# Optimization experiments

Hardware: AMD Instinct MI355X
Metric: run time of the kernel (lower is better)

## Reference

```python
import jax, jax.numpy as jnp
import numpy as np

EMBED_DIM = 512
NUM_HEADS = 8
TGT_LEN = 2048
SRC_LEN = 2048
BSZ = 4
W_SCALE = 0.02  # keep pre-softmax logits in a sane range


def setup_inputs() -> dict:
    key = jax.random.key(0)
    ks = jax.random.split(key, 13)
    E = EMBED_DIM
    inp = {
        "query": jax.random.normal(ks[0], (TGT_LEN, BSZ, E), jnp.float32),
        "key": jax.random.normal(ks[1], (SRC_LEN, BSZ, E), jnp.float32),
        "value": jax.random.normal(ks[2], (SRC_LEN, BSZ, E), jnp.float32),
        "attn_mask": jax.random.normal(ks[3], (TGT_LEN, SRC_LEN), jnp.float32),
        # Linear params, torch layout: W is [out, in], y = x @ W.T + b
        "Wq": jax.random.normal(ks[4], (E, E), jnp.float32) * W_SCALE,
        "bq": jax.random.normal(ks[5], (E,), jnp.float32) * W_SCALE,
        "Wk": jax.random.normal(ks[6], (E, E), jnp.float32) * W_SCALE,
        "bk": jax.random.normal(ks[7], (E,), jnp.float32) * W_SCALE,
        "Wv": jax.random.normal(ks[8], (E, E), jnp.float32) * W_SCALE,
        "bv": jax.random.normal(ks[9], (E,), jnp.float32) * W_SCALE,
        "Wo": jax.random.normal(ks[10], (E, E), jnp.float32) * W_SCALE,
        "bo": jax.random.normal(ks[11], (E,), jnp.float32) * W_SCALE,
    }
    return inp


def reference(query, key, value, attn_mask, Wq, bq, Wk, bk, Wv, bv, Wo, bo):
    # QAT quant/dequant stubs are identity in float math; dropout p=0 (eval) is identity.
    T, B, E = query.shape
    S = key.shape[0]
    H = NUM_HEADS
    hd = E // H
    scale = hd ** (-0.5)

    q = query @ Wq.T + bq            # [T, B, E]
    k = key @ Wk.T + bk              # [S, B, E]
    v = value @ Wv.T + bv            # [S, B, E]

    q = q.reshape(T, B, H, hd) * scale
    k = k.reshape(S, B, H, hd)
    v = v.reshape(S, B, H, hd)

    # scores: [B, H, T, S]
    scores = jnp.einsum("tbhd,sbhd->bhts", q, k)
    scores = scores + attn_mask[None, None, :, :]  # mask_add.add (float mask)
    attn = jax.nn.softmax(scores, axis=-1)         # SegmentLUTSoftmax == softmax in float

    out = jnp.einsum("bhts,sbhd->tbhd", attn, v).reshape(T, B, E)
    out = out @ Wo.T + bo                          # out_proj

    # need_weights=True, average_attn_weights=True: mean over heads -> [B, T, S]
    attn_weights = jnp.sum(attn, axis=1) * (1.0 / H)
    return out, attn_weights
```

## Files before the change

### kernel.cpp

```cpp
#include <hip/hip_runtime.h>
#include <hip/hip_bf16.h>

#define T_LEN 2048
#define S_LEN 2048
#define BSZ   4
#define EMB   512
#define NHEAD 8
#define HDIM  64

using bf16x8 = __attribute__((ext_vector_type(8))) short;
using f32x4  = __attribute__((ext_vector_type(4))) float;

static __device__ __forceinline__ unsigned short f2bf(float x) {
    __hip_bfloat16 h = __float2bfloat16(x);
    return *reinterpret_cast<unsigned short*>(&h);
}
static __device__ __forceinline__ float bf2f(unsigned short u) {
    __hip_bfloat16 h;
    *reinterpret_cast<unsigned short*>(&h) = u;
    return __bfloat162float(h);
}
static __device__ __forceinline__ unsigned int pk2(float a, float b) {
    return (unsigned)f2bf(a) | ((unsigned)f2bf(b) << 16);
}

__global__ __launch_bounds__(256) void convert_w4(
    const float* __restrict__ W0, const float* __restrict__ W1,
    const float* __restrict__ W2, const float* __restrict__ W3,
    unsigned short* __restrict__ Hi, unsigned short* __restrict__ Lo, int n4)
{
    const int z = blockIdx.y;
    const float* X = (z == 0) ? W0 : (z == 1) ? W1 : (z == 2) ? W2 : W3;
    unsigned short* H = Hi + (size_t)z * (size_t)EMB * EMB;
    unsigned short* L = Lo + (size_t)z * (size_t)EMB * EMB;
    const int stride = gridDim.x * 256;
    for (int i = blockIdx.x * 256 + threadIdx.x; i < n4; i += stride) {
        float4 v = ((const float4*)X)[i];
        unsigned short h0 = f2bf(v.x), h1 = f2bf(v.y), h2 = f2bf(v.z), h3 = f2bf(v.w);
        uint2 ph, pg;
        ph.x = (unsigned)h0 | ((unsigned)h1 << 16);
        ph.y = (unsigned)h2 | ((unsigned)h3 << 16);
        pg.x = pk2(v.x - bf2f(h0), v.y - bf2f(h1));
        pg.y = pk2(v.z - bf2f(h2), v.w - bf2f(h3));
        ((uint2*)H)[i] = ph;
        ((uint2*)L)[i] = pg;
    }
}

template <int MODE, bool XF32>
__global__ __launch_bounds__(256) void proj_mfma(
    const float* __restrict__ Xf,
    const unsigned short* __restrict__ Xhi, const unsigned short* __restrict__ Xlo,
    const unsigned short* __restrict__ Whi, const unsigned short* __restrict__ Wlo,
    const float* __restrict__ bias,
    float* __restrict__ Yf, unsigned short* __restrict__ Yhi, float scale)
{
    const int n0 = blockIdx.x * 64;
    const int m0 = blockIdx.y * 64;

    __shared__ unsigned short whs[64 * 64];
    __shared__ unsigned short wls[64 * 64];
    __shared__ unsigned short xhs[XF32 ? 64 * 64 : 1];
    __shared__ unsigned short xls[XF32 ? 64 * 64 : 1];

    const int tid = threadIdx.x;
    const int w   = tid >> 6;
    const int l   = tid & 63;
    const int l4  = l >> 4, l15 = l & 15;
    const int sw  = (l & 7) << 4;
    char* whsb = (char*)whs;
    char* wlsb = (char*)wls;
    char* xhsb = (char*)xhs;
    char* xlsb = (char*)xls;

    const int srow = tid >> 2;
    const int schk = tid & 3;
    const size_t wbase = (size_t)(n0 + srow) * 512 + schk * 16;
    const int stw = (srow * 128 + schk * 32) ^ ((srow & 7) << 4);

    f32x4 acc[4];
    #pragma unroll
    for (int nb = 0; nb < 4; ++nb) { f32x4 z = {0.f, 0.f, 0.f, 0.f}; acc[nb] = z; }

    uint4 wh0 = *(const uint4*)(Whi + wbase);
    uint4 wh1 = *(const uint4*)(Whi + wbase + 8);
    uint4 wl0 = *(const uint4*)(Wlo + wbase);
    uint4 wl1 = *(const uint4*)(Wlo + wbase + 8);

    const size_t xfbase = (size_t)(m0 + srow) * 512 + schk * 16;
    const size_t xbase  = (size_t)(m0 + w * 16 + l15) * 512 + l4 * 8;
    float4 xp0, xp1, xp2, xp3;
    bf16x8 ah0, ah1, al0, al1;
    if constexpr (XF32) {
        xp0 = *(const float4*)(Xf + xfbase);
        xp1 = *(const float4*)(Xf + xfbase + 4);
        xp2 = *(const float4*)(Xf + xfbase + 8);
        xp3 = *(const float4*)(Xf + xfbase + 12);
    } else {
        ah0 = *(const bf16x8*)(Xhi + xbase);
        ah1 = *(const bf16x8*)(Xhi + xbase + 32);
        al0 = *(const bf16x8*)(Xlo + xbase);
        al1 = *(const bf16x8*)(Xlo + xbase + 32);
    }

    for (int c = 0; c < 8; ++c) {
        __syncthreads();
        *(uint4*)(whsb + stw)        = wh0;
        *(uint4*)(whsb + (stw ^ 16)) = wh1;
        *(uint4*)(wlsb + stw)        = wl0;
        *(uint4*)(wlsb + (stw ^ 16)) = wl1;
        if constexpr (XF32) {
            uint4 H0, H1, L0, L1;
            H0.x = pk2(xp0.x, xp0.y); H0.y = pk2(xp0.z, xp0.w);
            H0.z = pk2(xp1.x, xp1.y); H0.w = pk2(xp1.z, xp1.w);
            H1.x = pk2(xp2.x, xp2.y); H1.y = pk2(xp2.z, xp2.w);
            H1.z = pk2(xp3.x, xp3.y); H1.w = pk2(xp3.z, xp3.w);
            L0.x = pk2(xp0.x - bf2f(f2bf(xp0.x)), xp0.y - bf2f(f2bf(xp0.y)));
            L0.y = pk2(xp0.z - bf2f(f2bf(xp0.z)), xp0.w - bf2f(f2bf(xp0.w)));
            L0.z = pk2(xp1.x - bf2f(f2bf(xp1.x)), xp1.y - bf2f(f2bf(xp1.y)));
            L0.w = pk2(xp1.z - bf2f(f2bf(xp1.z)), xp1.w - bf2f(f2bf(xp1.w)));
            L1.x = pk2(xp2.x - bf2f(f2bf(xp2.x)), xp2.y - bf2f(f2bf(xp2.y)));
            L1.y = pk2(xp2.z - bf2f(f2bf(xp2.z)), xp2.w - bf2f(f2bf(xp2.w)));
            L1.z = pk2(xp3.x - bf2f(f2bf(xp3.x)), xp3.y - bf2f(f2bf(xp3.y)));
            L1.w = pk2(xp3.z - bf2f(f2bf(xp3.z)), xp3.w - bf2f(f2bf(xp3.w)));
            *(uint4*)(xhsb + stw)        = H0;
            *(uint4*)(xhsb + (stw ^ 16)) = H1;
            *(uint4*)(xlsb + stw)        = L0;
            *(uint4*)(xlsb + (stw ^ 16)) = L1;
        }
        __syncthreads();

        bf16x8 cah[2], cal[2];
        if constexpr (XF32) {
            #pragma unroll
            for (int kc = 0; kc < 2; ++kc) {
                const int aoff = (((w * 16 + l15) * 128) + kc * 64 + l4 * 16) ^ sw;
                cah[kc] = *(const bf16x8*)(xhsb + aoff);
                cal[kc] = *(const bf16x8*)(xlsb + aoff);
            }
        } else {
            cah[0] = ah0; cah[1] = ah1; cal[0] = al0; cal[1] = al1;
        }

        if (c < 7) {
            const size_t wb2 = wbase + (size_t)(c + 1) * 64;
            wh0 = *(const uint4*)(Whi + wb2);
            wh1 = *(const uint4*)(Whi + wb2 + 8);
            wl0 = *(const uint4*)(Wlo + wb2);
            wl1 = *(const uint4*)(Wlo + wb2 + 8);
            if constexpr (XF32) {
                const size_t xb2 = xfbase + (size_t)(c + 1) * 64;
                xp0 = *(const float4*)(Xf + xb2);
                xp1 = *(const float4*)(Xf + xb2 + 4);
                xp2 = *(const float4*)(Xf + xb2 + 8);
                xp3 = *(const float4*)(Xf + xb2 + 12);
            } else {
                const size_t xb2 = xbase + (size_t)(c + 1) * 64;
                ah0 = *(const bf16x8*)(Xhi + xb2);
                ah1 = *(const bf16x8*)(Xhi + xb2 + 32);
                al0 = *(const bf16x8*)(Xlo + xb2);
                al1 = *(const bf16x8*)(Xlo + xb2 + 32);
            }
        }

        #pragma unroll
        for (int kc = 0; kc < 2; ++kc) {
            #pragma unroll
            for (int nb = 0; nb < 4; ++nb) {
                const int off = (((nb * 16 + l15) * 128) + kc * 64 + l4 * 16) ^ sw;
                bf16x8 bh = *(const bf16x8*)(whsb + off);
                bf16x8 bl = *(const bf16x8*)(wlsb + off);
                acc[nb] = __builtin_amdgcn_mfma_f32_16x16x32_bf16(cah[kc], bh, acc[nb], 0, 0, 0);
                acc[nb] = __builtin_amdgcn_mfma_f32_16x16x32_bf16(cah[kc], bl, acc[nb], 0, 0, 0);
                acc[nb] = __builtin_amdgcn_mfma_f32_16x16x32_bf16(cal[kc], bh, acc[nb], 0, 0, 0);
            }
        }
    }

    #pragma unroll
    for (int nb = 0; nb < 4; ++nb)
        #pragma unroll
        for (int r = 0; r < 4; ++r) {
            const int m = m0 + w * 16 + l4 * 4 + r;
            const int n = n0 + nb * 16 + l15;
            const float y = (acc[nb][r] + bias[n]) * scale;
            const size_t idx = (size_t)m * 512 + n;
            if constexpr (MODE == 0) Yf[idx] = y;
            else                     Yhi[idx] = f2bf(y);
        }
}

__global__ __launch_bounds__(256) void transpose_v(const unsigned short* __restrict__ V,
                                                   unsigned short* __restrict__ Vt)
{
    const int s0 = blockIdx.x * 64;
    const int h  = blockIdx.y, b = blockIdx.z;
    __shared__ unsigned short tile[64][72];
    const int tid = threadIdx.x;
    {
        const int r = tid >> 2, c = (tid & 3) * 16;
        const unsigned short* src = V + ((size_t)(s0 + r) * BSZ + b) * EMB + h * HDIM + c;
        uint4 u0 = *(const uint4*)(src);
        uint4 u1 = *(const uint4*)(src + 8);
        *(uint4*)&tile[r][c]     = u0;
        *(uint4*)&tile[r][c + 8] = u1;
    }
    __syncthreads();
    {
        const int d = tid >> 2, sg = tid & 3;
        unsigned int w_[8];
        #pragma unroll
        for (int j = 0; j < 8; ++j) {
            unsigned int lo = tile[sg * 16 + 2 * j][d];
            unsigned int hi = tile[sg * 16 + 2 * j + 1][d];
            w_[j] = lo | (hi << 16);
        }
        uint4 o0 = {w_[0], w_[1], w_[2], w_[3]};
        uint4 o1 = {w_[4], w_[5], w_[6], w_[7]};
        unsigned short* dst = Vt + ((size_t)(b * NHEAD + h) * HDIM + d) * S_LEN + s0 + sg * 16;
        *(uint4*)dst       = o0;
        *(uint4*)(dst + 8) = o1;
    }
}

__global__ __launch_bounds__(256) void flash_fwd_mfma(
    const unsigned short* __restrict__ Qbf, const unsigned short* __restrict__ Kbf,
    const unsigned short* __restrict__ Vt,  const float* __restrict__ mask,
    unsigned short* __restrict__ Ohi, unsigned short* __restrict__ Olo,
    float* __restrict__ Lout)
{
    const int tt0 = blockIdx.x * 128;
    const int h   = blockIdx.y, b = blockIdx.z;

    __shared__ unsigned short ks[64 * 64];
    __shared__ unsigned short vs[64 * 64];
    __shared__ unsigned short pl[4][2][16 * 64];

    const int tid = threadIdx.x;
    const int w   = tid >> 6;
    const int l   = tid & 63;
    const int l4  = l >> 4, l15 = l & 15;
    const int sw  = (l & 7) << 4;

    char* ksb = (char*)ks;
    char* vsb = (char*)vs;
    char* pb_[2] = {(char*)pl[w][0], (char*)pl[w][1]};

    bf16x8 qf[2][2];
    #pragma unroll
    for (int a = 0; a < 2; ++a) {
        const int t = tt0 + w * 32 + a * 16 + l15;
        const unsigned short* qp = Qbf + ((size_t)t * BSZ + b) * EMB + h * HDIM + l4 * 8;
        qf[a][0] = *(const bf16x8*)(qp);
        qf[a][1] = *(const bf16x8*)(qp + 32);
    }

    f32x4 oacc[2][4];
    #pragma unroll
    for (int a = 0; a < 2; ++a)
        #pragma unroll
        for (int nb = 0; nb < 4; ++nb) { f32x4 z = {0.f, 0.f, 0.f, 0.f}; oacc[a][nb] = z; }
    float lsum[2] = {0.f, 0.f};

    const int srow = tid >> 2;
    const int schk = tid & 3;
    const unsigned short* kcol = Kbf + (size_t)b * EMB + h * HDIM + schk * 16;
    const unsigned short* vrow = Vt + ((size_t)(b * NHEAD + h) * HDIM + srow) * S_LEN + schk * 16;
    const int stw = (srow * 128 + schk * 32) ^ ((srow & 7) << 4);

    const float* mrowp[2];
    #pragma unroll
    for (int a = 0; a < 2; ++a)
        mrowp[a] = mask + (size_t)(tt0 + w * 32 + a * 16 + l15) * S_LEN + l4 * 4;

    const unsigned short* kp0 = kcol + (size_t)srow * BSZ * EMB;
    uint4 ka0 = *(const uint4*)(kp0);
    uint4 ka1 = *(const uint4*)(kp0 + 8);
    uint4 va0 = *(const uint4*)(vrow);
    uint4 va1 = *(const uint4*)(vrow + 8);

    for (int s0 = 0; s0 < S_LEN; s0 += 64) {
        __syncthreads();
        *(uint4*)(ksb + stw)        = ka0;
        *(uint4*)(ksb + (stw ^ 16)) = ka1;
        *(uint4*)(vsb + stw)        = va0;
        *(uint4*)(vsb + (stw ^ 16)) = va1;
        __syncthreads();

        if (s0 + 64 < S_LEN) {
            const unsigned short* kp2 = kcol + (size_t)(s0 + 64 + srow) * BSZ * EMB;
            ka0 = *(const uint4*)(kp2);
            ka1 = *(const uint4*)(kp2 + 8);
            va0 = *(const uint4*)(vrow + s0 + 64);
            va1 = *(const uint4*)(vrow + s0 + 64 + 8);
        }

        f32x4 sacc[2][4];
        #pragma unroll
        for (int a = 0; a < 2; ++a)
            #pragma unroll
            for (int nb = 0; nb < 4; ++nb) { f32x4 z = {0.f, 0.f, 0.f, 0.f}; sacc[a][nb] = z; }
        #pragma unroll
        for (int kc = 0; kc < 2; ++kc) {
            #pragma unroll
            for (int nb = 0; nb < 4; ++nb) {
                const int off = (((nb * 16 + l15) * 128) + kc * 64 + l4 * 16) ^ sw;
                bf16x8 kf = *(const bf16x8*)(ksb + off);
                sacc[0][nb] = __builtin_amdgcn_mfma_f32_16x16x32_bf16(kf, qf[0][kc], sacc[0][nb], 0, 0, 0);
                sacc[1][nb] = __builtin_amdgcn_mfma_f32_16x16x32_bf16(kf, qf[1][kc], sacc[1][nb], 0, 0, 0);
            }
        }

        #pragma unroll
        for (int a = 0; a < 2; ++a) {
            char* pw = pb_[a];
            #pragma unroll
            for (int nb = 0; nb < 4; ++nb) {
                float4 mk = *(const float4*)(mrowp[a] + s0 + nb * 16);
                const float p0 = __expf(sacc[a][nb][0] + mk.x);
                const float p1 = __expf(sacc[a][nb][1] + mk.y);
                const float p2 = __expf(sacc[a][nb][2] + mk.z);
                const float p3 = __expf(sacc[a][nb][3] + mk.w);
                lsum[a] += (p0 + p1) + (p2 + p3);
                uint2 pk;
                pk.x = pk2(p0, p1);
                pk.y = pk2(p2, p3);
                *(uint2*)(pw + ((l15 * 128 + nb * 32 + l4 * 8) ^ sw)) = pk;
            }
        }

        bf16x8 pa[2][2];
        #pragma unroll
        for (int a = 0; a < 2; ++a) {
            pa[a][0] = *(const bf16x8*)(pb_[a] + ((l15 * 128 + l4 * 16) ^ sw));
            pa[a][1] = *(const bf16x8*)(pb_[a] + ((l15 * 128 + 64 + l4 * 16) ^ sw));
        }
        #pragma unroll
        for (int nb = 0; nb < 4; ++nb) {
            const int off0 = (((nb * 16 + l15) * 128) + l4 * 16) ^ sw;
            bf16x8 vf0 = *(const bf16x8*)(vsb + off0);
            bf16x8 vf1 = *(const bf16x8*)(vsb + (off0 ^ 64));
            oacc[0][nb] = __builtin_amdgcn_mfma_f32_16x16x32_bf16(pa[0][0], vf0, oacc[0][nb], 0, 0, 0);
            oacc[0][nb] = __builtin_amdgcn_mfma_f32_16x16x32_bf16(pa[0][1], vf1, oacc[0][nb], 0, 0, 0);
            oacc[1][nb] = __builtin_amdgcn_mfma_f32_16x16x32_bf16(pa[1][0], vf0, oacc[1][nb], 0, 0, 0);
            oacc[1][nb] = __builtin_amdgcn_mfma_f32_16x16x32_bf16(pa[1][1], vf1, oacc[1][nb], 0, 0, 0);
        }
    }

    #pragma unroll
    for (int a = 0; a < 2; ++a) {
        float lfull = lsum[a];
        lfull += __shfl_xor(lfull, 16);
        lfull += __shfl_xor(lfull, 32);
        float linv[4];
        #pragma unroll
        for (int r = 0; r < 4; ++r)
            linv[r] = 1.0f / __shfl(lfull, l4 * 4 + r);

        #pragma unroll
        for (int nb = 0; nb < 4; ++nb)
            #pragma unroll
            for (int r = 0; r < 4; ++r) {
                const int t = tt0 + w * 32 + a * 16 + l4 * 4 + r;
                const size_t idx = ((size_t)t * BSZ + b) * EMB + h * HDIM + nb * 16 + l15;
                const float y = oacc[a][nb][r] * linv[r];
                const unsigned short hi = f2bf(y);
                Ohi[idx] = hi;
                Olo[idx] = f2bf(y - bf2f(hi));
            }
        if (l < 16)
            Lout[((size_t)b * NHEAD + h) * T_LEN + tt0 + w * 32 + a * 16 + l] = lfull;
    }
}

__global__ __launch_bounds__(256) void attn_weights_mfma(
    const unsigned short* __restrict__ Qhi, const unsigned short* __restrict__ Khi,
    const float* __restrict__ mask, const float* __restrict__ Lin,
    float* __restrict__ Wout)
{
    const int tt0 = blockIdx.x * 128;
    const int ss0 = blockIdx.y * 64;
    const int b   = blockIdx.z;

    __shared__ unsigned short khs[64 * 64];
    __shared__ float lls[NHEAD][128];

    const int tid = threadIdx.x;
    const int w   = tid >> 6;
    const int l   = tid & 63;
    const int l4  = l >> 4, l15 = l & 15;
    const int sw  = (l & 7) << 4;
    char* khsb = (char*)khs;

    for (int i = tid; i < NHEAD * 128; i += 256) {
        const int hh = i >> 7, t2 = i & 127;
        lls[hh][t2] = 1.0f / Lin[(size_t)(b * NHEAD + hh) * T_LEN + tt0 + t2];
    }

    float4 msk[2][4];
    #pragma unroll
    for (int a = 0; a < 2; ++a) {
        const float* mrowp = mask + (size_t)(tt0 + w * 32 + a * 16 + l15) * S_LEN + ss0 + l4 * 4;
        #pragma unroll
        for (int nb = 0; nb < 4; ++nb) msk[a][nb] = *(const float4*)(mrowp + nb * 16);
    }

    float4 wacc[2][4] = {};

    const int srow = tid >> 2;
    const int schk = tid & 3;
    const size_t kbase = ((size_t)(ss0 + srow) * BSZ + b) * EMB + schk * 16;
    const int stw = (srow * 128 + schk * 32) ^ ((srow & 7) << 4);
    size_t qbase[2];
    #pragma unroll
    for (int a = 0; a < 2; ++a)
        qbase[a] = ((size_t)(tt0 + w * 32 + a * 16 + l15) * BSZ + b) * EMB + l4 * 8;

    uint4 kh0 = *(const uint4*)(Khi + kbase);
    uint4 kh1 = *(const uint4*)(Khi + kbase + 8);

    for (int h = 0; h < NHEAD; ++h) {
        __syncthreads();
        *(uint4*)(khsb + stw)        = kh0;
        *(uint4*)(khsb + (stw ^ 16)) = kh1;
        __syncthreads();

        if (h < NHEAD - 1) {
            kh0 = *(const uint4*)(Khi + kbase + (h + 1) * HDIM);
            kh1 = *(const uint4*)(Khi + kbase + (h + 1) * HDIM + 8);
        }

        bf16x8 qh[2][2];
        #pragma unroll
        for (int a = 0; a < 2; ++a) {
            qh[a][0] = *(const bf16x8*)(Qhi + qbase[a] + h * HDIM);
            qh[a][1] = *(const bf16x8*)(Qhi + qbase[a] + h * HDIM + 32);
        }

        f32x4 sacc[2][4];
        #pragma unroll
        for (int a = 0; a < 2; ++a)
            #pragma unroll
            for (int nb = 0; nb < 4; ++nb) { f32x4 z = {0.f, 0.f, 0.f, 0.f}; sacc[a][nb] = z; }
        #pragma unroll
        for (int kc = 0; kc < 2; ++kc) {
            #pragma unroll
            for (int nb = 0; nb < 4; ++nb) {
                const int off = (((nb * 16 + l15) * 128) + kc * 64 + l4 * 16) ^ sw;
                bf16x8 kf = *(const bf16x8*)(khsb + off);
                sacc[0][nb] = __builtin_amdgcn_mfma_f32_16x16x32_bf16(kf, qh[0][kc], sacc[0][nb], 0, 0, 0);
                sacc[1][nb] = __builtin_amdgcn_mfma_f32_16x16x32_bf16(kf, qh[1][kc], sacc[1][nb], 0, 0, 0);
            }
        }

        #pragma unroll
        for (int a = 0; a < 2; ++a) {
            const float lh = lls[h][w * 32 + a * 16 + l15];
            #pragma unroll
            for (int nb = 0; nb < 4; ++nb) {
                wacc[a][nb].x += __expf(sacc[a][nb][0] + msk[a][nb].x) * lh;
                wacc[a][nb].y += __expf(sacc[a][nb][1] + msk[a][nb].y) * lh;
                wacc[a][nb].z += __expf(sacc[a][nb][2] + msk[a][nb].z) * lh;
                wacc[a][nb].w += __expf(sacc[a][nb][3] + msk[a][nb].w) * lh;
            }
        }
    }

    #pragma unroll
    for (int a = 0; a < 2; ++a) {
        float* orow = Wout + ((size_t)b * T_LEN + tt0 + w * 32 + a * 16 + l15) * S_LEN + ss0 + l4 * 4;
        #pragma unroll
        for (int nb = 0; nb < 4; ++nb) {
            float4 o = {wacc[a][nb].x * (1.0f / NHEAD), wacc[a][nb].y * (1.0f / NHEAD),
                        wacc[a][nb].z * (1.0f / NHEAD), wacc[a][nb].w * (1.0f / NHEAD)};
            *(float4*)(orow + nb * 16) = o;
        }
    }
}

extern "C" void kernel_launch(void* const* d_in, const int* in_sizes, int n_in,
                              void* d_out, int out_size, void* d_ws, size_t ws_size,
                              hipStream_t stream)
{
    const float* query = (const float*)d_in[0];
    const float* key   = (const float*)d_in[1];
    const float* value = (const float*)d_in[2];
    const float* mask  = (const float*)d_in[3];
    const float* Wq    = (const float*)d_in[4];
    const float* bq    = (const float*)d_in[5];
    const float* Wk    = (const float*)d_in[6];
    const float* bk    = (const float*)d_in[7];
    const float* Wv    = (const float*)d_in[8];
    const float* bv    = (const float*)d_in[9];
    const float* Wo    = (const float*)d_in[10];
    const float* bo    = (const float*)d_in[11];

    float* out = (float*)d_out;

    const size_t NQKV = (size_t)T_LEN * BSZ * EMB;
    const size_t NW   = (size_t)EMB * EMB;

    unsigned short* qhi = (unsigned short*)d_ws;
    unsigned short* khi = qhi + NQKV;
    unsigned short* vhi = khi + NQKV;
    unsigned short* whb = vhi + NQKV;
    unsigned short* wlb = whb + 4 * NW;
    float* lb = (float*)(wlb + 4 * NW);

    unsigned short* wqh = whb + 0 * NW, *wql = wlb + 0 * NW;
    unsigned short* wkh = whb + 1 * NW, *wkl = wlb + 1 * NW;
    unsigned short* wvh = whb + 2 * NW, *wvl = wlb + 2 * NW;
    unsigned short* woh = whb + 3 * NW, *wol = wlb + 3 * NW;

    unsigned short* vt  = (unsigned short*)(out + NQKV);
    unsigned short* cxh = (unsigned short*)(out + NQKV + 3000000);
    unsigned short* cxl = (unsigned short*)(out + NQKV + 6000000);

    const dim3 gproj(8, 128);

    convert_w4<<<dim3(64, 4), 256, 0, stream>>>(Wq, Wk, Wv, Wo, whb, wlb, (int)(NW / 4));

    proj_mfma<2, true><<<gproj, 256, 0, stream>>>(query, nullptr, nullptr, wqh, wql, bq,
                                                  nullptr, qhi, 0.125f);
    proj_mfma<2, true><<<gproj, 256, 0, stream>>>(key, nullptr, nullptr, wkh, wkl, bk,
                                                  nullptr, khi, 1.0f);
    proj_mfma<2, true><<<gproj, 256, 0, stream>>>(value, nullptr, nullptr, wvh, wvl, bv,
                                                  nullptr, vhi, 1.0f);

    transpose_v<<<dim3(S_LEN / 64, NHEAD, BSZ), 256, 0, stream>>>(vhi, vt);

    flash_fwd_mfma<<<dim3(T_LEN / 128, NHEAD, BSZ), 256, 0, stream>>>(
        qhi, khi, vt, mask, cxh, cxl, lb);

    proj_mfma<0, false><<<gproj, 256, 0, stream>>>(nullptr, cxh, cxl, woh, wol, bo,
                                                   out, nullptr, 1.0f);

    attn_weights_mfma<<<dim3(T_LEN / 128, S_LEN / 64, BSZ), 256, 0, stream>>>(
        qhi, khi, mask, lb, out + NQKV);
}
```

Measured before the change: 257.7 us.

## Split flash attention over key halves and drop split-bf16 for QKV projections

Result: slower. 287.1 us (+11.4%).

```diff
diff --git a/kernel.cpp b/kernel.cpp
--- a/kernel.cpp
+++ b/kernel.cpp
@@ -7,6 +7,8 @@
 #define EMB   512
 #define NHEAD 8
 #define HDIM  64
+#define NSPLIT 2
+#define SHALF (S_LEN / NSPLIT)
 
 using bf16x8 = __attribute__((ext_vector_type(8))) short;
 using f32x4  = __attribute__((ext_vector_type(4))) float;
@@ -47,7 +49,7 @@
     }
 }
 
-template <int MODE, bool XF32>
+template <int MODE, bool XF32, bool SPLIT>
 __global__ __launch_bounds__(256) void proj_mfma(
     const float* __restrict__ Xf,
     const unsigned short* __restrict__ Xhi, const unsigned short* __restrict__ Xlo,
@@ -59,9 +61,9 @@
     const int m0 = blockIdx.y * 64;
 
     __shared__ unsigned short whs[64 * 64];
-    __shared__ unsigned short wls[64 * 64];
+    __shared__ unsigned short wls[SPLIT ? 64 * 64 : 1];
     __shared__ unsigned short xhs[XF32 ? 64 * 64 : 1];
-    __shared__ unsigned short xls[XF32 ? 64 * 64 : 1];
+    __shared__ unsigned short xls[(XF32 && SPLIT) ? 64 * 64 : 1];
 
     const int tid = threadIdx.x;
     const int w   = tid >> 6;
@@ -84,8 +86,11 @@
 
     uint4 wh0 = *(const uint4*)(Whi + wbase);
     uint4 wh1 = *(const uint4*)(Whi + wbase + 8);
-    uint4 wl0 = *(const uint4*)(Wlo + wbase);
-    uint4 wl1 = *(const uint4*)(Wlo + wbase + 8);
+    uint4 wl0, wl1;
+    if constexpr (SPLIT) {
+        wl0 = *(const uint4*)(Wlo + wbase);
+        wl1 = *(const uint4*)(Wlo + wbase + 8);
+    }
 
     const size_t xfbase = (size_t)(m0 + srow) * 512 + schk * 16;
     const size_t xbase  = (size_t)(m0 + w * 16 + l15) * 512 + l4 * 8;
@@ -99,34 +104,41 @@
     } else {
         ah0 = *(const bf16x8*)(Xhi + xbase);
         ah1 = *(const bf16x8*)(Xhi + xbase + 32);
-        al0 = *(const bf16x8*)(Xlo + xbase);
-        al1 = *(const bf16x8*)(Xlo + xbase + 32);
+        if constexpr (SPLIT) {
+            al0 = *(const bf16x8*)(Xlo + xbase);
+            al1 = *(const bf16x8*)(Xlo + xbase + 32);
+        }
     }
 
     for (int c = 0; c < 8; ++c) {
         __syncthreads();
         *(uint4*)(whsb + stw)        = wh0;
         *(uint4*)(whsb + (stw ^ 16)) = wh1;
-        *(uint4*)(wlsb + stw)        = wl0;
-        *(uint4*)(wlsb + (stw ^ 16)) = wl1;
+        if constexpr (SPLIT) {
+            *(uint4*)(wlsb + stw)        = wl0;
+            *(uint4*)(wlsb + (stw ^ 16)) = wl1;
+        }
         if constexpr (XF32) {
-            uint4 H0, H1, L0, L1;
+            uint4 H0, H1;
             H0.x = pk2(xp0.x, xp0.y); H0.y = pk2(xp0.z, xp0.w);
             H0.z = pk2(xp1.x, xp1.y); H0.w = pk2(xp1.z, xp1.w);
             H1.x = pk2(xp2.x, xp2.y); H1.y = pk2(xp2.z, xp2.w);
             H1.z = pk2(xp3.x, xp3.y); H1.w = pk2(xp3.z, xp3.w);
-            L0.x = pk2(xp0.x - bf2f(f2bf(xp0.x)), xp0.y - bf2f(f2bf(xp0.y)));
-            L0.y = pk2(xp0.z - bf2f(f2bf(xp0.z)), xp0.w - bf2f(f2bf(xp0.w)));
-            L0.z = pk2(xp1.x - bf2f(f2bf(xp1.x)), xp1.y - bf2f(f2bf(xp1.y)));
-            L0.w = pk2(xp1.z - bf2f(f2bf(xp1.z)), xp1.w - bf2f(f2bf(xp1.w)));
-            L1.x = pk2(xp2.x - bf2f(f2bf(xp2.x)), xp2.y - bf2f(f2bf(xp2.y)));
-            L1.y = pk2(xp2.z - bf2f(f2bf(xp2.z)), xp2.w - bf2f(f2bf(xp2.w)));
-            L1.z = pk2(xp3.x - bf2f(f2bf(xp3.x)), xp3.y - bf2f(f2bf(xp3.y)));
-            L1.w = pk2(xp3.z - bf2f(f2bf(xp3.z)), xp3.w - bf2f(f2bf(xp3.w)));
             *(uint4*)(xhsb + stw)        = H0;
             *(uint4*)(xhsb + (stw ^ 16)) = H1;
-            *(uint4*)(xlsb + stw)        = L0;
-            *(uint4*)(xlsb + (stw ^ 16)) = L1;
+            if constexpr (SPLIT) {
+                uint4 L0, L1;
+                L0.x = pk2(xp0.x - bf2f(f2bf(xp0.x)), xp0.y - bf2f(f2bf(xp0.y)));
+                L0.y = pk2(xp0.z - bf2f(f2bf(xp0.z)), xp0.w - bf2f(f2bf(xp0.w)));
+                L0.z = pk2(xp1.x - bf2f(f2bf(xp1.x)), xp1.y - bf2f(f2bf(xp1.y)));
+                L0.w = pk2(xp1.z - bf2f(f2bf(xp1.z)), xp1.w - bf2f(f2bf(xp1.w)));
+                L1.x = pk2(xp2.x - bf2f(f2bf(xp2.x)), xp2.y - bf2f(f2bf(xp2.y)));
+                L1.y = pk2(xp2.z - bf2f(f2bf(xp2.z)), xp2.w - bf2f(f2bf(xp2.w)));
+                L1.z = pk2(xp3.x - bf2f(f2bf(xp3.x)), xp3.y - bf2f(f2bf(xp3.y)));
+                L1.w = pk2(xp3.z - bf2f(f2bf(xp3.z)), xp3.w - bf2f(f2bf(xp3.w)));
+                *(uint4*)(xlsb + stw)        = L0;
+                *(uint4*)(xlsb + (stw ^ 16)) = L1;
+            }
         }
         __syncthreads();
 
@@ -136,18 +148,21 @@
             for (int kc = 0; kc < 2; ++kc) {
                 const int aoff = (((w * 16 + l15) * 128) + kc * 64 + l4 * 16) ^ sw;
                 cah[kc] = *(const bf16x8*)(xhsb + aoff);
-                cal[kc] = *(const bf16x8*)(xlsb + aoff);
+                if constexpr (SPLIT) cal[kc] = *(const bf16x8*)(xlsb + aoff);
             }
         } else {
-            cah[0] = ah0; cah[1] = ah1; cal[0] = al0; cal[1] = al1;
+            cah[0] = ah0; cah[1] = ah1;
+            if constexpr (SPLIT) { cal[0] = al0; cal[1] = al1; }
         }
 
         if (c < 7) {
             const size_t wb2 = wbase + (size_t)(c + 1) * 64;
             wh0 = *(const uint4*)(Whi + wb2);
             wh1 = *(const uint4*)(Whi + wb2 + 8);
-            wl0 = *(const uint4*)(Wlo + wb2);
-            wl1 = *(const uint4*)(Wlo + wb2 + 8);
+            if constexpr (SPLIT) {
+                wl0 = *(const uint4*)(Wlo + wb2);
+                wl1 = *(const uint4*)(Wlo + wb2 + 8);
+            }
             if constexpr (XF32) {
                 const size_t xb2 = xfbase + (size_t)(c + 1) * 64;
                 xp0 = *(const float4*)(Xf + xb2);
@@ -158,8 +173,10 @@
                 const size_t xb2 = xbase + (size_t)(c + 1) * 64;
                 ah0 = *(const bf16x8*)(Xhi + xb2);
                 ah1 = *(const bf16x8*)(Xhi + xb2 + 32);
-                al0 = *(const bf16x8*)(Xlo + xb2);
-                al1 = *(const bf16x8*)(Xlo + xb2 + 32);
+                if constexpr (SPLIT) {
+                    al0 = *(const bf16x8*)(Xlo + xb2);
+                    al1 = *(const bf16x8*)(Xlo + xb2 + 32);
+                }
             }
         }
 
@@ -169,10 +186,12 @@
             for (int nb = 0; nb < 4; ++nb) {
                 const int off = (((nb * 16 + l15) * 128) + kc * 64 + l4 * 16) ^ sw;
                 bf16x8 bh = *(const bf16x8*)(whsb + off);
-                bf16x8 bl = *(const bf16x8*)(wlsb + off);
                 acc[nb] = __builtin_amdgcn_mfma_f32_16x16x32_bf16(cah[kc], bh, acc[nb], 0, 0, 0);
-                acc[nb] = __builtin_amdgcn_mfma_f32_16x16x32_bf16(cah[kc], bl, acc[nb], 0, 0, 0);
-                acc[nb] = __builtin_amdgcn_mfma_f32_16x16x32_bf16(cal[kc], bh, acc[nb], 0, 0, 0);
+                if constexpr (SPLIT) {
+                    bf16x8 bl = *(const bf16x8*)(wlsb + off);
+                    acc[nb] = __builtin_amdgcn_mfma_f32_16x16x32_bf16(cah[kc], bl, acc[nb], 0, 0, 0);
+                    acc[nb] = __builtin_amdgcn_mfma_f32_16x16x32_bf16(cal[kc], bh, acc[nb], 0, 0, 0);
+                }
             }
         }
     }
@@ -226,11 +245,12 @@
 __global__ __launch_bounds__(256) void flash_fwd_mfma(
     const unsigned short* __restrict__ Qbf, const unsigned short* __restrict__ Kbf,
     const unsigned short* __restrict__ Vt,  const float* __restrict__ mask,
-    unsigned short* __restrict__ Ohi, unsigned short* __restrict__ Olo,
-    float* __restrict__ Lout)
-{
-    const int tt0 = blockIdx.x * 128;
-    const int h   = blockIdx.y, b = blockIdx.z;
+    float* __restrict__ Opart, float* __restrict__ Lpart)
+{
+    const int split = blockIdx.x & (NSPLIT - 1);
+    const int tt0   = (blockIdx.x / NSPLIT) * 128;
+    const int h     = blockIdx.y, b = blockIdx.z;
+    const int sbase = split * SHALF;
 
     __shared__ unsigned short ks[64 * 64];
     __shared__ unsigned short vs[64 * 64];
@@ -273,13 +293,13 @@
     for (int a = 0; a < 2; ++a)
         mrowp[a] = mask + (size_t)(tt0 + w * 32 + a * 16 + l15) * S_LEN + l4 * 4;
 
-    const unsigned short* kp0 = kcol + (size_t)srow * BSZ * EMB;
+    const unsigned short* kp0 = kcol + (size_t)(sbase + srow) * BSZ * EMB;
     uint4 ka0 = *(const uint4*)(kp0);
     uint4 ka1 = *(const uint4*)(kp0 + 8);
-    uint4 va0 = *(const uint4*)(vrow);
-    uint4 va1 = *(const uint4*)(vrow + 8);
-
-    for (int s0 = 0; s0 < S_LEN; s0 += 64) {
+    uint4 va0 = *(const uint4*)(vrow + sbase);
+    uint4 va1 = *(const uint4*)(vrow + sbase + 8);
+
+    for (int s0 = sbase; s0 < sbase + SHALF; s0 += 64) {
         __syncthreads();
         *(uint4*)(ksb + stw)        = ka0;
         *(uint4*)(ksb + (stw ^ 16)) = ka1;
@@ -287,7 +307,7 @@
         *(uint4*)(vsb + (stw ^ 16)) = va1;
         __syncthreads();
 
-        if (s0 + 64 < S_LEN) {
+        if (s0 + 64 < sbase + SHALF) {
             const unsigned short* kp2 = kcol + (size_t)(s0 + 64 + srow) * BSZ * EMB;
             ka0 = *(const uint4*)(kp2);
             ka1 = *(const uint4*)(kp2 + 8);
@@ -347,36 +367,68 @@
         }
     }
 
+    float* Op = Opart + (size_t)split * T_LEN * BSZ * EMB;
+    float* Lp = Lpart + (size_t)split * BSZ * NHEAD * T_LEN;
     #pragma unroll
     for (int a = 0; a < 2; ++a) {
         float lfull = lsum[a];
         lfull += __shfl_xor(lfull, 16);
         lfull += __shfl_xor(lfull, 32);
-        float linv[4];
-        #pragma unroll
-        for (int r = 0; r < 4; ++r)
-            linv[r] = 1.0f / __shfl(lfull, l4 * 4 + r);
-
         #pragma unroll
         for (int nb = 0; nb < 4; ++nb)
             #pragma unroll
             for (int r = 0; r < 4; ++r) {
                 const int t = tt0 + w * 32 + a * 16 + l4 * 4 + r;
-                const size_t idx = ((size_t)t * BSZ + b) * EMB + h * HDIM + nb * 16 + l15;
-                const float y = oacc[a][nb][r] * linv[r];
-                const unsigned short hi = f2bf(y);
-                Ohi[idx] = hi;
-                Olo[idx] = f2bf(y - bf2f(hi));
+                Op[((size_t)t * BSZ + b) * EMB + h * HDIM + nb * 16 + l15] = oacc[a][nb][r];
             }
         if (l < 16)
-            Lout[((size_t)b * NHEAD + h) * T_LEN + tt0 + w * 32 + a * 16 + l] = lfull;
-    }
+            Lp[((size_t)b * NHEAD + h) * T_LEN + tt0 + w * 32 + a * 16 + l] = lfull;
+    }
+}
+
+__global__ __launch_bounds__(256) void merge_o(
+    const float* __restrict__ P0, const float* __restrict__ P1,
+    const float* __restrict__ L0, const float* __restrict__ L1,
+    unsigned short* __restrict__ Ohi, unsigned short* __restrict__ Olo)
+{
+    const int gid = blockIdx.x * 256 + threadIdx.x;
+    const int row = gid >> 3;
+    const int chunk = gid & 7;
+    const int hh = row & 7, tb = row >> 3, b = tb & 3, t = tb >> 2;
+    const size_t lidx = ((size_t)b * NHEAD + hh) * T_LEN + t;
+    const float linv = 1.0f / (L0[lidx] + L1[lidx]);
+    const size_t off = (size_t)row * 64 + chunk * 8;
+
+    float4 a0 = *(const float4*)(P0 + off);
+    float4 a1 = *(const float4*)(P0 + off + 4);
+    float4 b0 = *(const float4*)(P1 + off);
+    float4 b1 = *(const float4*)(P1 + off + 4);
+    float y[8];
+    y[0] = (a0.x + b0.x) * linv; y[1] = (a0.y + b0.y) * linv;
+    y[2] = (a0.z + b0.z) * linv; y[3] = (a0.w + b0.w) * linv;
+    y[4] = (a1.x + b1.x) * linv; y[5] = (a1.y + b1.y) * linv;
+    y[6] = (a1.z + b1.z) * linv; y[7] = (a1.w + b1.w) * linv;
+
+    unsigned short h_[8];
+    uint4 H, L;
+    #pragma unroll
+    for (int j = 0; j < 8; ++j) h_[j] = f2bf(y[j]);
+    H.x = (unsigned)h_[0] | ((unsigned)h_[1] << 16);
+    H.y = (unsigned)h_[2] | ((unsigned)h_[3] << 16);
+    H.z = (unsigned)h_[4] | ((unsigned)h_[5] << 16);
+    H.w = (unsigned)h_[6] | ((unsigned)h_[7] << 16);
+    L.x = pk2(y[0] - bf2f(h_[0]), y[1] - bf2f(h_[1]));
+    L.y = pk2(y[2] - bf2f(h_[2]), y[3] - bf2f(h_[3]));
+    L.z = pk2(y[4] - bf2f(h_[4]), y[5] - bf2f(h_[5]));
+    L.w = pk2(y[6] - bf2f(h_[6]), y[7] - bf2f(h_[7]));
+    *(uint4*)(Ohi + off) = H;
+    *(uint4*)(Olo + off) = L;
 }
 
 __global__ __launch_bounds__(256) void attn_weights_mfma(
     const unsigned short* __restrict__ Qhi, const unsigned short* __restrict__ Khi,
-    const float* __restrict__ mask, const float* __restrict__ Lin,
-    float* __restrict__ Wout)
+    const float* __restrict__ mask, const float* __restrict__ L0,
+    const float* __restrict__ L1, float* __restrict__ Wout)
 {
     const int tt0 = blockIdx.x * 128;
     const int ss0 = blockIdx.y * 64;
@@ -394,7 +446,8 @@
 
     for (int i = tid; i < NHEAD * 128; i += 256) {
         const int hh = i >> 7, t2 = i & 127;
-        lls[hh][t2] = 1.0f / Lin[(size_t)(b * NHEAD + hh) * T_LEN + tt0 + t2];
+        const size_t idx = (size_t)(b * NHEAD + hh) * T_LEN + tt0 + t2;
+        lls[hh][t2] = 1.0f / (L0[idx] + L1[idx]);
     }
 
     float4 msk[2][4];
@@ -499,42 +552,48 @@
 
     const size_t NQKV = (size_t)T_LEN * BSZ * EMB;
     const size_t NW   = (size_t)EMB * EMB;
+    const size_t NBHT = (size_t)BSZ * NHEAD * T_LEN;
 
     unsigned short* qhi = (unsigned short*)d_ws;
     unsigned short* khi = qhi + NQKV;
     unsigned short* vhi = khi + NQKV;
     unsigned short* whb = vhi + NQKV;
     unsigned short* wlb = whb + 4 * NW;
-    float* lb = (float*)(wlb + 4 * NW);
-
-    unsigned short* wqh = whb + 0 * NW, *wql = wlb + 0 * NW;
-    unsigned short* wkh = whb + 1 * NW, *wkl = wlb + 1 * NW;
-    unsigned short* wvh = whb + 2 * NW, *wvl = wlb + 2 * NW;
+    float* lp0 = (float*)(wlb + 4 * NW);
+    float* lp1 = lp0 + NBHT;
+
+    unsigned short* wqh = whb + 0 * NW;
+    unsigned short* wkh = whb + 1 * NW;
+    unsigned short* wvh = whb + 2 * NW;
     unsigned short* woh = whb + 3 * NW, *wol = wlb + 3 * NW;
 
-    unsigned short* vt  = (unsigned short*)(out + NQKV);
-    unsigned short* cxh = (unsigned short*)(out + NQKV + 3000000);
-    unsigned short* cxl = (unsigned short*)(out + NQKV + 6000000);
+    float* op0 = out + NQKV;
+    float* op1 = op0 + NQKV;
+    unsigned short* vt  = (unsigned short*)(op1 + NQKV);
+    unsigned short* cxh = vt + NQKV;
+    unsigned short* cxl = cxh + NQKV;
 
     const dim3 gproj(8, 128);
 
     convert_w4<<<dim3(64, 4), 256, 0, stream>>>(Wq, Wk, Wv, Wo, whb, wlb, (int)(NW / 4));
 
-    proj_mfma<2, true><<<gproj, 256, 0, stream>>>(query, nullptr, nullptr, wqh, wql, bq,
-                                                  nullptr, qhi, 0.125f);
-    proj_mfma<2, true><<<gproj, 256, 0, stream>>>(key, nullptr, nullptr, wkh, wkl, bk,
-                                                  nullptr, khi, 1.0f);
-    proj_mfma<2, true><<<gproj, 256, 0, stream>>>(value, nullptr, nullptr, wvh, wvl, bv,
-                                                  nullptr, vhi, 1.0f);
+    proj_mfma<2, true, false><<<gproj, 256, 0, stream>>>(query, nullptr, nullptr, wqh, nullptr,
+                                                         bq, nullptr, qhi, 0.125f);
+    proj_mfma<2, true, false><<<gproj, 256, 0, stream>>>(key, nullptr, nullptr, wkh, nullptr,
+                                                         bk, nullptr, khi, 1.0f);
+    proj_mfma<2, true, false><<<gproj, 256, 0, stream>>>(value, nullptr, nullptr, wvh, nullptr,
+                                                         bv, nullptr, vhi, 1.0f);
 
     transpose_v<<<dim3(S_LEN / 64, NHEAD, BSZ), 256, 0, stream>>>(vhi, vt);
 
-    flash_fwd_mfma<<<dim3(T_LEN / 128, NHEAD, BSZ), 256, 0, stream>>>(
-        qhi, khi, vt, mask, cxh, cxl, lb);
-
-    proj_mfma<0, false><<<gproj, 256, 0, stream>>>(nullptr, cxh, cxl, woh, wol, bo,
-                                                   out, nullptr, 1.0f);
+    flash_fwd_mfma<<<dim3((T_LEN / 128) * NSPLIT, NHEAD, BSZ), 256, 0, stream>>>(
+        qhi, khi, vt, mask, op0, lp0);
+
+    merge_o<<<(int)(NQKV / 8 / 256), 256, 0, stream>>>(op0, op1, lp0, lp1, cxh, cxl);
+
+    proj_mfma<0, false, true><<<gproj, 256, 0, stream>>>(nullptr, cxh, cxl, woh, wol, bo,
+                                                         out, nullptr, 1.0f);
 
     attn_weights_mfma<<<dim3(T_LEN / 128, S_LEN / 64, BSZ), 256, 0, stream>>>(
-        qhi, khi, mask, lb, out + NQKV);
-}
+        qhi, khi, mask, lp0, lp1, out + NQKV);
+}
```
